# Performance work log

Hardware: AMD Instinct MI355X
Metric: run time of the kernel (lower is better)

Reference implementation:

```python
import jax, jax.numpy as jnp
import numpy as np

STRIDE = 4
PAD = 12  # kernel_size // 2 = 25 // 2


def setup_inputs() -> dict:
    key = jax.random.key(0)
    k1, k2 = jax.random.split(key)
    x = jax.random.normal(k1, (16, 3, 224, 224), dtype=jnp.float32)
    # Gabor filter bank weight [out_channels, 1, k, k]; random stands in for
    # the fixed (non-learned) gabor_kernel init.
    weight = jax.random.normal(k2, (512, 1, 25, 25), dtype=jnp.float32)
    return {"x": x, "weight": weight}


def reference(x, weight):
    # Original: python loop over input channels, each convolved with the SAME
    # [O,1,k,k] bank, results concatenated -> [B, C, O, H', W'].
    # Equivalent single conv: fold channel dim into batch.
    B, C, H, W = x.shape
    O = weight.shape[0]
    xm = x.reshape(B * C, 1, H, W)
    out = jax.lax.conv_general_dilated(
        xm, weight,
        window_strides=(STRIDE, STRIDE),
        padding=[(PAD, PAD), (PAD, PAD)],
        dimension_numbers=("NCHW", "OIHW", "NCHW"),
    )  # [B*C, O, H', W']
    Hp, Wp = out.shape[2], out.shape[3]
    return out.reshape(B, C, O, Hp, Wp)
```

## Files before the change

kernel.cpp:

```cpp
#include <hip/hip_runtime.h>
#include <stdint.h>


typedef __attribute__((ext_vector_type(8))) short short8v;
typedef __attribute__((ext_vector_type(4))) short short4v;
typedef __attribute__((ext_vector_type(4))) float float4v;

namespace {
constexpr int H = 224, W = 224, OC = 512, KS = 25, ST = 4, PD = 12;
constexpr int HO = 56, WO = 56;
constexpr int TCH = 128;
constexpr int TOY = 4;
constexpr int IR  = (TOY - 1) * ST + KS;
constexpr int IC  = (WO - 1) * ST + 32;
constexpr int ISTR = 260;
constexpr int KXP = 32;
constexpr int WSTR = 40;
constexpr int CHT = OC / TCH;
constexpr int OYT = HO / TOY;
constexpr int NIMG = 48;
constexpr int NB = NIMG * CHT * OYT;
constexpr size_t W2_BYTES = (size_t)KS * OC * KXP * sizeof(short);
}

__device__ __forceinline__ short f2bf(float f) {
    uint32_t u = __float_as_uint(f);
    u += 0x7fffu + ((u >> 16) & 1u);
    return (short)(u >> 16);
}

__global__ void prep_w(const float* __restrict__ wt, short* __restrict__ w2) {
    int idx = blockIdx.x * 256 + threadIdx.x;
    if (idx >= KS * OC * KXP) return;
    int kx = idx & 31;
    int t  = idx >> 5;
    int ch = t & (OC - 1);
    int ky = t >> 9;
    float v = (kx < KS) ? wt[ch * (KS * KS) + ky * KS + kx] : 0.0f;
    w2[idx] = f2bf(v);
}

__global__ __launch_bounds__(256, 2)
void gabor_mfma(const float* __restrict__ x,
                const short* __restrict__ w2,
                float* __restrict__ out) {
    __shared__ __align__(16) short in_lds[IR * ISTR];

    const int tid = threadIdx.x;
    int bid = blockIdx.x;
    const int oyg = bid % OYT; bid /= OYT;
    const int cht = bid % CHT; bid /= CHT;
    const int img = bid;

    const int oy0 = oyg * TOY;
    const int cbase = cht * TCH;
    const int iy0 = oy0 * ST - PD;
    const float* __restrict__ xin = x + (size_t)img * H * W;

    constexpr int ICP = IC / 2;
    for (int idx = tid; idx < IR * ICP; idx += 256) {
        int r = idx / ICP, cp = idx % ICP;
        int c = cp * 2;
        int iy = iy0 + r, ix = c - PD;
        float v0 = 0.0f, v1 = 0.0f;
        if ((unsigned)iy < (unsigned)H) {
            if ((unsigned)ix < (unsigned)W)       v0 = xin[iy * W + ix];
            if ((unsigned)(ix + 1) < (unsigned)W) v1 = xin[iy * W + ix + 1];
        }
        uint32_t pk = (uint32_t)(uint16_t)f2bf(v0) |
                      ((uint32_t)(uint16_t)f2bf(v1) << 16);
        *(uint32_t*)&in_lds[r * ISTR + c] = pk;
    }
    __syncthreads();

    const int lane = tid & 63;
    const int wid  = tid >> 6;
    const int wr = wid >> 1;
    const int wc = wid & 1;
    const int n = lane & 15;
    const int q = lane >> 4;
    const int brow0 = (wc * 2 + (n >> 3)) * ST;
    const int bcol  = (n & 7) * ST + q * 8;

    const short* __restrict__ w2b =
        w2 + (size_t)(cbase + wr * 64 + n) * KXP + q * 8;

    float4v acc[4][7];
    #pragma unroll
    for (int a = 0; a < 4; ++a)
        #pragma unroll
        for (int b = 0; b < 7; ++b)
            acc[a][b] = (float4v)0.0f;

    short8v A0[4], A1[4];

    auto loadA = [&](int ky, short8v* dst) {
        #pragma unroll
        for (int a = 0; a < 4; ++a)
            dst[a] = *(const short8v*)(w2b + (size_t)ky * (OC * KXP) + a * (16 * KXP));
    };

    auto body = [&](int ky, const short8v* A) {
        const short* __restrict__ inp = &in_lds[(brow0 + ky) * ISTR + bcol];
        short8v Bv[7];
        #pragma unroll
        for (int b = 0; b < 7; ++b) {
            const short* p = inp + b * 32;
            short4v lo = *(const short4v*)p;
            short4v hi = *(const short4v*)(p + 4);
            Bv[b] = __builtin_shufflevector(lo, hi, 0, 1, 2, 3, 4, 5, 6, 7);
        }
        #pragma unroll
        for (int b = 0; b < 7; ++b)
            #pragma unroll
            for (int a = 0; a < 4; ++a)
                acc[a][b] = __builtin_amdgcn_mfma_f32_16x16x32_bf16(A[a], Bv[b], acc[a][b], 0, 0, 0);
    };

    loadA(0, A0);
    for (int kk = 0; kk < 12; ++kk) {
        const int ky = kk * 2;
        loadA(ky + 1, A1);
        body(ky, A0);
        loadA(ky + 2, A0);
        body(ky + 1, A1);
    }
    body(24, A0);

    const int oy = oy0 + wc * 2 + (n >> 3);
    const int chb = cbase + wr * 64 + q * 4;
    #pragma unroll
    for (int a = 0; a < 4; ++a) {
        #pragma unroll
        for (int b = 0; b < 7; ++b) {
            const int ch = chb + a * 16;
            const int ox = b * 8 + (n & 7);
            float* op = out + (((size_t)img * OC + ch) * HO + oy) * WO + ox;
            float4v v = acc[a][b];
            op[0]            = v[0];
            op[HO * WO]      = v[1];
            op[2 * HO * WO]  = v[2];
            op[3 * HO * WO]  = v[3];
        }
    }
}

__device__ __forceinline__ void stage_w_fb(short* dst, const float* __restrict__ wsrc,
                                           int ky, int tid) {
    #pragma unroll
    for (int i = 0; i < (TCH * KXP) / 256; ++i) {
        int idx = tid + i * 256;
        int ch = idx >> 5, kx = idx & 31;
        float v = (kx < KS) ? wsrc[ch * (KS * KS) + ky * KS + kx] : 0.0f;
        dst[ch * WSTR + kx] = f2bf(v);
    }
}

__global__ __launch_bounds__(256, 2)
void gabor_mfma_fb(const float* __restrict__ x,
                   const float* __restrict__ wt,
                   float* __restrict__ out) {
    __shared__ __align__(16) short in_lds[IR * ISTR];
    __shared__ __align__(16) short w_lds[2][TCH * WSTR];

    const int tid = threadIdx.x;
    int bid = blockIdx.x;
    const int oyg = bid % OYT; bid /= OYT;
    const int cht = bid % CHT; bid /= CHT;
    const int img = bid;

    const int oy0 = oyg * TOY;
    const int cbase = cht * TCH;
    const int iy0 = oy0 * ST - PD;
    const float* __restrict__ xin = x + (size_t)img * H * W;
    const float* __restrict__ wsrc = wt + (size_t)cbase * (KS * KS);

    for (int idx = tid; idx < IR * IC; idx += 256) {
        int r = idx / IC, c = idx % IC;
        int iy = iy0 + r, ix = c - PD;
        float v = 0.0f;
        if ((unsigned)iy < (unsigned)H && (unsigned)ix < (unsigned)W)
            v = xin[iy * W + ix];
        in_lds[r * ISTR + c] = f2bf(v);
    }
    stage_w_fb(w_lds[0], wsrc, 0, tid);
    __syncthreads();

    const int lane = tid & 63;
    const int wid  = tid >> 6;
    const int wr = wid >> 1;
    const int wc = wid & 1;
    const int n = lane & 15;
    const int q = lane >> 4;
    const int brow0 = (wc * 2 + (n >> 3)) * ST;
    const int bcol  = (n & 7) * ST + q * 8;
    const int awoff = (wr * 64 + n) * WSTR + q * 8;

    float4v acc[4][7];
    #pragma unroll
    for (int a = 0; a < 4; ++a)
        #pragma unroll
        for (int b = 0; b < 7; ++b)
            acc[a][b] = (float4v)0.0f;

    for (int ky = 0; ky < KS; ++ky) {
        const int cur = ky & 1;
        if (ky + 1 < KS) stage_w_fb(w_lds[cur ^ 1], wsrc, ky + 1, tid);

        const short* __restrict__ inp = &in_lds[(brow0 + ky) * ISTR + bcol];
        short8v Bv[7];
        #pragma unroll
        for (int b = 0; b < 7; ++b) {
            const short* p = inp + b * 32;
            short4v lo = *(const short4v*)p;
            short4v hi = *(const short4v*)(p + 4);
            Bv[b] = __builtin_shufflevector(lo, hi, 0, 1, 2, 3, 4, 5, 6, 7);
        }
        const short* __restrict__ wp = &w_lds[cur][awoff];
        #pragma unroll
        for (int a = 0; a < 4; ++a) {
            short8v A = *(const short8v*)(wp + a * 16 * WSTR);
            #pragma unroll
            for (int b = 0; b < 7; ++b)
                acc[a][b] = __builtin_amdgcn_mfma_f32_16x16x32_bf16(A, Bv[b], acc[a][b], 0, 0, 0);
        }
        __syncthreads();
    }

    const int oy = oy0 + wc * 2 + (n >> 3);
    const int chb = cbase + wr * 64 + q * 4;
    #pragma unroll
    for (int a = 0; a < 4; ++a) {
        #pragma unroll
        for (int b = 0; b < 7; ++b) {
            const int ch = chb + a * 16;
            const int ox = b * 8 + (n & 7);
            float* op = out + (((size_t)img * OC + ch) * HO + oy) * WO + ox;
            float4v v = acc[a][b];
            op[0]            = v[0];
            op[HO * WO]      = v[1];
            op[2 * HO * WO]  = v[2];
            op[3 * HO * WO]  = v[3];
        }
    }
}

extern "C" void kernel_launch(void* const* d_in, const int* in_sizes, int n_in,
                              void* d_out, int out_size, void* d_ws, size_t ws_size,
                              hipStream_t stream) {
    const float* x  = (const float*)d_in[0];
    const float* wt = (const float*)d_in[1];
    float* out = (float*)d_out;
    (void)in_sizes; (void)n_in; (void)out_size;

    if (d_ws != nullptr && ws_size >= W2_BYTES) {
        short* w2 = (short*)d_ws;
        const int prep_total = KS * OC * KXP;
        prep_w<<<(prep_total + 255) / 256, 256, 0, stream>>>(wt, w2);
        gabor_mfma<<<NB, 256, 0, stream>>>(x, w2, out);
    } else {
        gabor_mfma_fb<<<NB, 256, 0, stream>>>(x, wt, out);
    }
}
```

Baseline: 422.1 us.

## Pre-pad input to bf16 in workspace and stage tiles via direct global-to-LDS loads

Adds a prep_x kernel that converts the input to a zero-padded bf16 image in workspace. The main kernel can then copy its input tile straight into LDS with 16-byte global_load_lds, replacing the per-block bounds-checked fp32 load and convert. It also reorders block IDs round-robin across 8 groups, and double-buffers the B fragments from LDS along with A in a fully unrolled ky loop. The cost is an extra kernel launch and an extra round trip of the image through workspace, plus more register pressure.

Measured after the change: 378.7 us. 1.11x faster.

```diff
diff --git a/kernel.cpp b/kernel.cpp
--- a/kernel.cpp
+++ b/kernel.cpp
@@ -12,21 +12,33 @@
 constexpr int TCH = 128;
 constexpr int TOY = 4;
 constexpr int IR  = (TOY - 1) * ST + KS;
-constexpr int IC  = (WO - 1) * ST + 32;
-constexpr int ISTR = 260;
+constexpr int IRP = 38;
+constexpr int ISTR = 256;
 constexpr int KXP = 32;
-constexpr int WSTR = 40;
 constexpr int CHT = OC / TCH;
 constexpr int OYT = HO / TOY;
 constexpr int NIMG = 48;
 constexpr int NB = NIMG * CHT * OYT;
+constexpr int XPH = 248, XPW = 256;
 constexpr size_t W2_BYTES = (size_t)KS * OC * KXP * sizeof(short);
+constexpr size_t XP_BYTES = (size_t)NIMG * XPH * XPW * sizeof(short);
+constexpr size_t WS_NEED  = W2_BYTES + XP_BYTES;
+constexpr int IC  = (WO - 1) * ST + 32;
+constexpr int ISTR_FB = 260;
+constexpr int WSTR = 40;
 }
 
 __device__ __forceinline__ short f2bf(float f) {
     uint32_t u = __float_as_uint(f);
     u += 0x7fffu + ((u >> 16) & 1u);
     return (short)(u >> 16);
+}
+
+__device__ __forceinline__ void gload_lds16(const void* gsrc, void* ldst) {
+    __builtin_amdgcn_global_load_lds(
+        (const __attribute__((address_space(1))) uint32_t*)gsrc,
+        (__attribute__((address_space(3))) uint32_t*)ldst,
+        16, 0, 0);
 }
 
 __global__ void prep_w(const float* __restrict__ wt, short* __restrict__ w2) {
@@ -40,38 +52,46 @@
     w2[idx] = f2bf(v);
 }
 
+__global__ void prep_x(const float* __restrict__ x, short* __restrict__ xp) {
+    int idx = blockIdx.x * 256 + threadIdx.x;
+    constexpr int total = NIMG * XPH * (XPW / 2);
+    if (idx >= total) return;
+    int cp  = idx & (XPW / 2 - 1);
+    int t   = idx >> 7;
+    int g   = t % XPH;
+    int img = t / XPH;
+    int c = cp * 2;
+    int iy = g - PD, ix = c - PD;
+    float v0 = 0.0f, v1 = 0.0f;
+    if ((unsigned)iy < (unsigned)H) {
+        const float* row = x + ((size_t)img * H + iy) * W;
+        if ((unsigned)ix < (unsigned)W)       v0 = row[ix];
+        if ((unsigned)(ix + 1) < (unsigned)W) v1 = row[ix + 1];
+    }
+    uint32_t pk = (uint32_t)(uint16_t)f2bf(v0) |
+                  ((uint32_t)(uint16_t)f2bf(v1) << 16);
+    *(uint32_t*)&xp[((size_t)img * XPH + g) * XPW + c] = pk;
+}
+
 __global__ __launch_bounds__(256, 2)
-void gabor_mfma(const float* __restrict__ x,
-                const short* __restrict__ w2,
+void gabor_mfma(const short* __restrict__ w2,
+                const short* __restrict__ xp,
                 float* __restrict__ out) {
-    __shared__ __align__(16) short in_lds[IR * ISTR];
+    __shared__ __align__(16) short in_lds[IRP * ISTR];
 
     const int tid = threadIdx.x;
-    int bid = blockIdx.x;
+    int bid = (blockIdx.x % 8) * (NB / 8) + blockIdx.x / 8;
     const int oyg = bid % OYT; bid /= OYT;
     const int cht = bid % CHT; bid /= CHT;
     const int img = bid;
 
     const int oy0 = oyg * TOY;
     const int cbase = cht * TCH;
-    const int iy0 = oy0 * ST - PD;
-    const float* __restrict__ xin = x + (size_t)img * H * W;
-
-    constexpr int ICP = IC / 2;
-    for (int idx = tid; idx < IR * ICP; idx += 256) {
-        int r = idx / ICP, cp = idx % ICP;
-        int c = cp * 2;
-        int iy = iy0 + r, ix = c - PD;
-        float v0 = 0.0f, v1 = 0.0f;
-        if ((unsigned)iy < (unsigned)H) {
-            if ((unsigned)ix < (unsigned)W)       v0 = xin[iy * W + ix];
-            if ((unsigned)(ix + 1) < (unsigned)W) v1 = xin[iy * W + ix + 1];
-        }
-        uint32_t pk = (uint32_t)(uint16_t)f2bf(v0) |
-                      ((uint32_t)(uint16_t)f2bf(v1) << 16);
-        *(uint32_t*)&in_lds[r * ISTR + c] = pk;
-    }
-    __syncthreads();
+
+    const char* xpb = (const char*)(xp + ((size_t)img * XPH + oy0 * ST) * XPW);
+    constexpr int CHUNKS = IRP * ISTR * 2 / 16;
+    for (int c = tid; c < CHUNKS; c += 256)
+        gload_lds16(xpb + (size_t)c * 16, (char*)in_lds + c * 16);
 
     const int lane = tid & 63;
     const int wid  = tid >> 6;
@@ -85,6 +105,16 @@
     const short* __restrict__ w2b =
         w2 + (size_t)(cbase + wr * 64 + n) * KXP + q * 8;
 
+    short8v A0[4], A1[4], B0[7], B1[7];
+
+    #pragma unroll
+    for (int a = 0; a < 4; ++a)
+        A0[a] = *(const short8v*)(w2b + a * (16 * KXP));
+
+    __syncthreads();
+
+    const short* __restrict__ inb = &in_lds[brow0 * ISTR + bcol];
+
     float4v acc[4][7];
     #pragma unroll
     for (int a = 0; a < 4; ++a)
@@ -92,40 +122,38 @@
         for (int b = 0; b < 7; ++b)
             acc[a][b] = (float4v)0.0f;
 
-    short8v A0[4], A1[4];
-
-    auto loadA = [&](int ky, short8v* dst) {
+    auto loadB = [&](int ky, short8v* Bd) {
+        const short* p = inb + ky * ISTR;
+        #pragma unroll
+        for (int b = 0; b < 7; ++b) {
+            short4v lo = *(const short4v*)(p + b * 32);
+            short4v hi = *(const short4v*)(p + b * 32 + 4);
+            Bd[b] = __builtin_shufflevector(lo, hi, 0, 1, 2, 3, 4, 5, 6, 7);
+        }
+    };
+    auto loadA = [&](int ky, short8v* Ad) {
+        const short* p = w2b + (size_t)ky * (OC * KXP);
         #pragma unroll
         for (int a = 0; a < 4; ++a)
-            dst[a] = *(const short8v*)(w2b + (size_t)ky * (OC * KXP) + a * (16 * KXP));
+            Ad[a] = *(const short8v*)(p + a * (16 * KXP));
     };
-
-    auto body = [&](int ky, const short8v* A) {
-        const short* __restrict__ inp = &in_lds[(brow0 + ky) * ISTR + bcol];
-        short8v Bv[7];
-        #pragma unroll
-        for (int b = 0; b < 7; ++b) {
-            const short* p = inp + b * 32;
-            short4v lo = *(const short4v*)p;
-            short4v hi = *(const short4v*)(p + 4);
-            Bv[b] = __builtin_shufflevector(lo, hi, 0, 1, 2, 3, 4, 5, 6, 7);
-        }
+    auto mma = [&](const short8v* Av, const short8v* Bv) {
         #pragma unroll
         for (int b = 0; b < 7; ++b)
             #pragma unroll
             for (int a = 0; a < 4; ++a)
-                acc[a][b] = __builtin_amdgcn_mfma_f32_16x16x32_bf16(A[a], Bv[b], acc[a][b], 0, 0, 0);
+                acc[a][b] = __builtin_amdgcn_mfma_f32_16x16x32_bf16(Av[a], Bv[b], acc[a][b], 0, 0, 0);
     };
 
-    loadA(0, A0);
-    for (int kk = 0; kk < 12; ++kk) {
-        const int ky = kk * 2;
-        loadA(ky + 1, A1);
-        body(ky, A0);
-        loadA(ky + 2, A0);
-        body(ky + 1, A1);
-    }
-    body(24, A0);
+    loadB(0, B0);
+    #pragma unroll
+    for (int ky = 0; ky < KS; ++ky) {
+        if (ky + 1 < KS) {
+            loadB(ky + 1, (ky & 1) ? B0 : B1);
+            loadA(ky + 1, (ky & 1) ? A0 : A1);
+        }
+        mma((ky & 1) ? A1 : A0, (ky & 1) ? B1 : B0);
+    }
 
     const int oy = oy0 + wc * 2 + (n >> 3);
     const int chb = cbase + wr * 64 + q * 4;
@@ -160,7 +188,7 @@
 void gabor_mfma_fb(const float* __restrict__ x,
                    const float* __restrict__ wt,
                    float* __restrict__ out) {
-    __shared__ __align__(16) short in_lds[IR * ISTR];
+    __shared__ __align__(16) short in_lds[IR * ISTR_FB];
     __shared__ __align__(16) short w_lds[2][TCH * WSTR];
 
     const int tid = threadIdx.x;
@@ -181,7 +209,7 @@
         float v = 0.0f;
         if ((unsigned)iy < (unsigned)H && (unsigned)ix < (unsigned)W)
             v = xin[iy * W + ix];
-        in_lds[r * ISTR + c] = f2bf(v);
+        in_lds[r * ISTR_FB + c] = f2bf(v);
     }
     stage_w_fb(w_lds[0], wsrc, 0, tid);
     __syncthreads();
@@ -207,7 +235,7 @@
         const int cur = ky & 1;
         if (ky + 1 < KS) stage_w_fb(w_lds[cur ^ 1], wsrc, ky + 1, tid);
 
-        const short* __restrict__ inp = &in_lds[(brow0 + ky) * ISTR + bcol];
+        const short* __restrict__ inp = &in_lds[(brow0 + ky) * ISTR_FB + bcol];
         short8v Bv[7];
         #pragma unroll
         for (int b = 0; b < 7; ++b) {
@@ -253,11 +281,14 @@
     float* out = (float*)d_out;
     (void)in_sizes; (void)n_in; (void)out_size;
 
-    if (d_ws != nullptr && ws_size >= W2_BYTES) {
+    if (d_ws != nullptr && ws_size >= WS_NEED) {
         short* w2 = (short*)d_ws;
-        const int prep_total = KS * OC * KXP;
-        prep_w<<<(prep_total + 255) / 256, 256, 0, stream>>>(wt, w2);
-        gabor_mfma<<<NB, 256, 0, stream>>>(x, w2, out);
+        short* xp = (short*)((char*)d_ws + W2_BYTES);
+        const int wtot = KS * OC * KXP;
+        const int xtot = NIMG * XPH * (XPW / 2);
+        prep_w<<<(wtot + 255) / 256, 256, 0, stream>>>(wt, w2);
+        prep_x<<<(xtot + 255) / 256, 256, 0, stream>>>(x, xp);
+        gabor_mfma<<<NB, 256, 0, stream>>>(w2, xp, out);
     } else {
         gabor_mfma_fb<<<NB, 256, 0, stream>>>(x, wt, out);
     }
```
